# Kernel optimization log

Hardware: AMD Instinct MI355X
Metric: run time of the kernel (lower is better)

Reference implementation:

```python
import jax, jax.numpy as jnp
import numpy as np

B, S, H = 2, 2048, 2048
NH, KVH, HD = 32, 8, 64
G = NH // KVH
BASE = 10000.0
SCALE = 1.0 / np.sqrt(HD).astype(np.float32)


def _rope_cache(seq_len, dim, base):
    inv_freq = 1.0 / (base ** (jnp.arange(0, dim, 2, dtype=jnp.float32) / dim))
    t = jnp.arange(seq_len, dtype=jnp.float32)
    freqs = jnp.outer(t, inv_freq)            # [S, HD/2]
    emb = jnp.concatenate([freqs, freqs], -1)  # [S, HD]
    return jnp.cos(emb), jnp.sin(emb)


def _rotate_half(x):
    x1, x2 = jnp.split(x, 2, axis=-1)
    return jnp.concatenate([-x2, x1], axis=-1)


def setup_inputs() -> dict:
    key = jax.random.key(0)
    ks = jax.random.split(key, 5)
    hidden_states = jax.random.normal(ks[0], (B, S, H), jnp.float32)
    # additive causal mask, broadcast over heads
    causal = jnp.tril(jnp.ones((S, S), dtype=bool))
    attention_mask = jnp.where(causal, 0.0, -1e9).astype(jnp.float32)[None, None]
    attention_mask = jnp.broadcast_to(attention_mask, (B, 1, S, S))
    position_ids = jnp.broadcast_to(jnp.arange(S, dtype=jnp.int32), (B, S))
    w = 0.02
    Wq = jax.random.normal(ks[1], (H, NH * HD), jnp.float32) * w
    Wk = jax.random.normal(ks[2], (H, KVH * HD), jnp.float32) * w
    Wv = jax.random.normal(ks[3], (H, KVH * HD), jnp.float32) * w
    Wo = jax.random.normal(ks[4], (NH * HD, H), jnp.float32) * w
    return {"hidden_states": hidden_states, "attention_mask": attention_mask,
            "position_ids": position_ids, "Wq": Wq, "Wk": Wk, "Wv": Wv, "Wo": Wo}


def reference(hidden_states, attention_mask, position_ids, Wq, Wk, Wv, Wo):
    b, s, _ = hidden_states.shape
    q = (hidden_states @ Wq).reshape(b, s, NH, HD).transpose(0, 2, 1, 3)   # [B,NH,S,HD]
    k = (hidden_states @ Wk).reshape(b, s, KVH, HD).transpose(0, 2, 1, 3)  # [B,KVH,S,HD]
    v = (hidden_states @ Wv).reshape(b, s, KVH, HD).transpose(0, 2, 1, 3)
    cos_c, sin_c = _rope_cache(s, HD, BASE)
    cos = cos_c[position_ids][:, None]  # [B,1,S,HD]
    sin = sin_c[position_ids][:, None]
    q = q * cos + _rotate_half(q) * sin
    k = k * cos + _rotate_half(k) * sin
    # GQA: grouped einsum == repeat_kv + matmul (same math, no KV duplication)
    qg = q.reshape(b, KVH, G, s, HD)
    scores = jnp.einsum('bkgsd,bktd->bkgst', qg, k) * SCALE  # [B,KVH,G,S,S]
    scores = scores + attention_mask[:, :, None]             # mask [B,1,1,S,S]
    probs = jax.nn.softmax(scores.astype(jnp.float32), axis=-1).astype(q.dtype)
    ctx = jnp.einsum('bkgst,bktd->bkgsd', probs, v)
    ctx = ctx.reshape(b, NH, s, HD).transpose(0, 2, 1, 3).reshape(b, s, NH * HD)
    return ctx @ Wo
```

## Files before the change

kernel.cpp:

```cpp
#include <hip/hip_runtime.h>
#include <hip/hip_bf16.h>

#define DB   2
#define DS   2048
#define DH   2048
#define DNH  32
#define DKVH 8
#define DHD  64
#define DM   4096
#define DNQKV 3072

typedef __attribute__((ext_vector_type(8))) short bf16x8;
typedef __attribute__((ext_vector_type(4))) float f32x4;
typedef __attribute__((ext_vector_type(8))) unsigned short us8;
typedef __attribute__((ext_vector_type(4))) unsigned short us4;
typedef __attribute__((ext_vector_type(2))) unsigned int u32x2;

__device__ __forceinline__ float b2f(unsigned short u) {
  unsigned int x = ((unsigned int)u) << 16;
  return __builtin_bit_cast(float, x);
}
__device__ __forceinline__ unsigned short f2b(float f) {
  unsigned int u = __builtin_bit_cast(unsigned int, f);
  return (unsigned short)((u + 0x8000u) >> 16);
}
__device__ __forceinline__ unsigned int cvt_pk_bf16(float lo, float hi) {
  unsigned int r;
  asm("v_cvt_pk_bf16_f32 %0, %1, %2" : "=v"(r) : "v"(lo), "v"(hi));
  return r;
}
__device__ __forceinline__ void async_copy16(void* lds, const void* g) {
  __builtin_amdgcn_global_load_lds((const __attribute__((address_space(1))) void*)g,
                                   (__attribute__((address_space(3))) void*)lds,
                                   16, 0, 0);
}

#define BARRIER() do { asm volatile("" ::: "memory"); __builtin_amdgcn_s_barrier(); asm volatile("" ::: "memory"); } while (0)
#define LGKM0()   asm volatile("s_waitcnt lgkmcnt(0)" ::: "memory")
#define WAITVM(n) asm volatile("s_waitcnt vmcnt(" #n ")" ::: "memory")
#define MFMA16(d, a, bb) (d) = __builtin_amdgcn_mfma_f32_16x16x32_bf16((a), (bb), (d), 0, 0, 0)

__device__ __forceinline__ int detect_inline(const unsigned short* __restrict__ w) {
  int t = threadIdx.x & 63;
  int trips = 0;
#pragma unroll
  for (int i = 0; i < 4; i++) {
    unsigned short u = w[t * 4 + i];
    int e = (u >> 7) & 0xFF;
    if (e >= 161 || (e <= 93 && e != 0)) trips++;
  }
#pragma unroll
  for (int off = 32; off > 0; off >>= 1) trips += __shfl_down(trips, off);
  return __shfl(trips, 0) >= 8;
}

__global__ __launch_bounds__(256)
void prep(const void* __restrict__ hs, const void* __restrict__ wq,
          const void* __restrict__ wk, const void* __restrict__ wv,
          const void* __restrict__ wo,
          unsigned short* __restrict__ xb, unsigned short* __restrict__ wtqkv,
          unsigned short* __restrict__ wto) {
  __shared__ float tile[32][33];
  int mode = detect_inline((const unsigned short*)wq);
  int bid = blockIdx.x;
  if (bid < 4096) {
    int i = (bid * 256 + threadIdx.x) * 8;
    if (mode) {
      const float* f = (const float*)hs;
      us8 o;
#pragma unroll
      for (int j = 0; j < 8; j++) o[j] = f2b(f[i + j]);
      *(us8*)&xb[i] = o;
    } else {
      *(us8*)&xb[i] = *(const us8*)((const unsigned short*)hs + i);
    }
    return;
  }
  const void* win; unsigned short* out; int C, bx, by;
  if (bid < 8192)       { int l = bid - 4096;  win = wq; out = wtqkv;                         C = 2048; bx = l & 63; by = l >> 6; }
  else if (bid < 9216)  { int l = bid - 8192;  win = wk; out = wtqkv + (size_t)2048 * 2048;   C = 512;  bx = l & 15; by = l >> 4; }
  else if (bid < 10240) { int l = bid - 9216;  win = wv; out = wtqkv + (size_t)2560 * 2048;   C = 512;  bx = l & 15; by = l >> 4; }
  else                  { int l = bid - 10240; win = wo; out = wto;                           C = 2048; bx = l & 63; by = l >> 6; }
  int c0 = bx * 32, r0 = by * 32;
  int tx = threadIdx.x & 31, ty = threadIdx.x >> 5;
  if (mode) {
    const float* f = (const float*)win;
    for (int i = ty; i < 32; i += 8) tile[i][tx] = f[(size_t)(r0 + i) * C + c0 + tx];
  } else {
    const unsigned short* bsrc = (const unsigned short*)win;
    for (int i = ty; i < 32; i += 8) tile[i][tx] = b2f(bsrc[(size_t)(r0 + i) * C + c0 + tx]);
  }
  __syncthreads();
  for (int i = ty; i < 32; i += 8) out[(size_t)(c0 + i) * 2048 + r0 + tx] = f2b(tile[tx][i]);
}

#define QSC 0.18033688011112042f

__global__ __launch_bounds__(512, 2)
void gemm_qkv(const unsigned short* __restrict__ A, const unsigned short* __restrict__ Bt,
              const int* __restrict__ pos_ids,
              unsigned short* __restrict__ qws, unsigned short* __restrict__ kws,
              unsigned short* __restrict__ vt) {
  __shared__ __align__(16) unsigned short sm[65536];
  int tid = threadIdx.x, lane = tid & 63, wave = tid >> 6;
  int wm = wave >> 2, wn = wave & 3;
  int quad = lane >> 4, l15 = lane & 15;

  int bid = blockIdx.x;
  int wg = (bid & 7) * 24 + (bid >> 3);
  int ty = wg / 12, tx = wg - ty * 12;
  size_t tm0 = (size_t)ty * 256, tn0 = (size_t)tx * 256;

  const unsigned short* Ab = A + tm0 * 2048;
  const unsigned short* Bb = Bt + tn0 * 2048;

  auto UA = [&](int bu, int kh) { return sm + (bu * 2 + kh) * 8192; };
  auto UB = [&](int bu, int kh) { return sm + 32768 + (bu * 2 + kh) * 8192; };

  int c0 = tid, c1 = tid + 512;
  int r0s = c0 >> 2, r1s = c1 >> 2;
  int cc0 = (c0 & 3) ^ ((r0s >> 1) & 3);
  int cc1 = (c1 & 3) ^ ((r1s >> 1) & 3);
  size_t ga0 = (size_t)r0s * 2048 + cc0 * 8;
  size_t ga1 = (size_t)r1s * 2048 + cc1 * 8;

  auto stA = [&](int t, int kh, int bu) {
    const unsigned short* s = Ab + (size_t)t * 64 + kh * 32;
    async_copy16(UA(bu, kh) + c0 * 8, s + ga0);
    async_copy16(UA(bu, kh) + c1 * 8, s + ga1);
  };
  auto stB = [&](int t, int kh, int bu) {
    const unsigned short* s = Bb + (size_t)t * 64 + kh * 32;
    async_copy16(UB(bu, kh) + c0 * 8, s + ga0);
    async_copy16(UB(bu, kh) + c1 * 8, s + ga1);
  };

  int rdoff = l15 * 32 + ((quad << 3) ^ (((l15 >> 1) & 3) << 3));

  f32x4 zero4 = {0.f, 0.f, 0.f, 0.f};
  f32x4 acc[8][4];
#pragma unroll
  for (int mi = 0; mi < 8; mi++)
#pragma unroll
    for (int ni = 0; ni < 4; ni++) acc[mi][ni] = zero4;

  stA(0, 0, 0); stB(0, 0, 0); stA(0, 1, 0); stB(0, 1, 0); stA(1, 0, 1); stB(1, 0, 1);
  WAITVM(8); BARRIER();

#pragma unroll 2
  for (int t = 0; t < 32; ++t) {
    int bu = t & 1, bn = bu ^ 1;
    int t1 = (t + 1 < 32) ? t + 1 : 31;
    int t2 = (t + 2 < 32) ? t + 2 : 31;
    bf16x8 af[8];
    const unsigned short* pA0 = UA(bu, 0) + wm * 4096 + rdoff;
    const unsigned short* pB0 = UB(bu, 0) + wn * 2048 + rdoff;
    const unsigned short* pA1 = UA(bu, 1) + wm * 4096 + rdoff;
    const unsigned short* pB1 = UB(bu, 1) + wn * 2048 + rdoff;

#pragma unroll
    for (int mi = 0; mi < 8; mi++) af[mi] = *(const bf16x8*)(pA0 + mi * 512);
    bf16x8 b0 = *(const bf16x8*)pB0;
    bf16x8 b1 = *(const bf16x8*)(pB0 + 512);
    stA(t1, 1, bn);
    BARRIER(); LGKM0();
    __builtin_amdgcn_s_setprio(1);
#pragma unroll
    for (int mi = 0; mi < 8; mi++) { MFMA16(acc[mi][0], af[mi], b0); MFMA16(acc[mi][1], af[mi], b1); }
    __builtin_amdgcn_s_setprio(0);
    BARRIER();

    bf16x8 b2 = *(const bf16x8*)(pB0 + 1024);
    bf16x8 b3 = *(const bf16x8*)(pB0 + 1536);
    stB(t1, 1, bn);
    BARRIER(); LGKM0();
    __builtin_amdgcn_s_setprio(1);
#pragma unroll
    for (int mi = 0; mi < 8; mi++) { MFMA16(acc[mi][2], af[mi], b2); MFMA16(acc[mi][3], af[mi], b3); }
    __builtin_amdgcn_s_setprio(0);
    WAITVM(8);
    BARRIER();

#pragma unroll
    for (int mi = 0; mi < 8; mi++) af[mi] = *(const bf16x8*)(pA1 + mi * 512);
    b0 = *(const bf16x8*)pB1;
    b1 = *(const bf16x8*)(pB1 + 512);
    stA(t2, 0, bu);
    BARRIER(); LGKM0();
    __builtin_amdgcn_s_setprio(1);
#pragma unroll
    for (int mi = 0; mi < 8; mi++) { MFMA16(acc[mi][0], af[mi], b0); MFMA16(acc[mi][1], af[mi], b1); }
    __builtin_amdgcn_s_setprio(0);
    BARRIER();

    b2 = *(const bf16x8*)(pB1 + 1024);
    b3 = *(const bf16x8*)(pB1 + 1536);
    stB(t2, 0, bu);
    BARRIER(); LGKM0();
    __builtin_amdgcn_s_setprio(1);
#pragma unroll
    for (int mi = 0; mi < 8; mi++) { MFMA16(acc[mi][2], af[mi], b2); MFMA16(acc[mi][3], af[mi], b3); }
    __builtin_amdgcn_s_setprio(0);
    WAITVM(8);
    BARRIER();
  }
  WAITVM(0);

  int hs = (int)(tn0 >> 6) + wn;
  if (hs < 40) {
    float sc = (hs < 32) ? QSC : 1.0f;
    unsigned short* dst0 = (hs < 32) ? qws : kws;
    int hh = (hs < 32) ? hs : (hs - 32);
    float invf0 = __expf(-(float)l15 * (9.210340371976184f / 32.0f));
    float invf1 = invf0 * 0.01f;
#pragma unroll
    for (int mi = 0; mi < 8; mi++)
#pragma unroll
      for (int r = 0; r < 4; r++) {
        size_t gr = tm0 + wm * 128 + mi * 16 + quad * 4 + r;
        int bb = (int)(gr >> 11), s = (int)(gr & 2047);
        float tpos = (float)pos_ids[gr];
        unsigned short* row = dst0 + ((size_t)(bb * ((hs < 32) ? DNH : DKVH) + hh) * DS + s) * DHD;
#pragma unroll
        for (int ni = 0; ni < 2; ni++) {
          float x1 = acc[mi][ni][r], x2 = acc[mi][ni + 2][r];
          float ang = tpos * (ni ? invf1 : invf0);
          float sn, cs;
          __sincosf(ang, &sn, &cs);
          int d = ni * 16 + l15;
          row[d]      = f2b((x1 * cs - x2 * sn) * sc);
          row[d + 32] = f2b((x2 * cs + x1 * sn) * sc);
        }
      }
  } else {
    int vh = hs - 40;
    int bb = (int)(tm0 >> 11);
    int s0 = (int)(tm0 & 2047) + wm * 128 + quad * 4;
#pragma unroll
    for (int mi = 0; mi < 8; mi++)
#pragma unroll
      for (int ni = 0; ni < 4; ni++) {
        int d = ni * 16 + l15;
        us4 o4;
#pragma unroll
        for (int r = 0; r < 4; r++) o4[r] = f2b(acc[mi][ni][r]);
        *(us4*)&vt[((size_t)(bb * DKVH + vh) * DHD + d) * DS + s0 + mi * 16] = o4;
      }
  }
}

__global__ __launch_bounds__(512, 2)
void gemm_out(const unsigned short* __restrict__ A, const unsigned short* __restrict__ Bt,
              unsigned short* __restrict__ Cb, float* __restrict__ Cf,
              const unsigned short* __restrict__ wqdet) {
  __shared__ __align__(16) unsigned short sm[49152];
  int tid = threadIdx.x, lane = tid & 63, wave = tid >> 6;
  int wm = wave >> 2, wn = wave & 3;
  int quad = lane >> 4, l15 = lane & 15;

  int bid = blockIdx.x;
  int wg = (bid & 7) * 32 + (bid >> 3);
  int ty = wg >> 3, tx = wg & 7;
  size_t tm0 = (size_t)ty * 128, tn0 = (size_t)tx * 256;

  const unsigned short* Ab = A + tm0 * 2048;
  const unsigned short* Bb = Bt + tn0 * 2048;

  auto UA = [&](int bu, int kh) { return sm + (bu * 2 + kh) * 4096; };
  auto UB = [&](int bu, int kh) { return sm + 16384 + (bu * 2 + kh) * 8192; };

  int c0 = tid, c1 = tid + 512;
  int r0s = c0 >> 2, r1s = c1 >> 2;
  int cc0 = (c0 & 3) ^ ((r0s >> 1) & 3);
  int cc1 = (c1 & 3) ^ ((r1s >> 1) & 3);
  size_t ga0 = (size_t)r0s * 2048 + cc0 * 8;
  size_t ga1 = (size_t)r1s * 2048 + cc1 * 8;

  auto stA = [&](int t, int kh, int bu) {
    const unsigned short* s = Ab + (size_t)t * 64 + kh * 32;
    async_copy16(UA(bu, kh) + c0 * 8, s + ga0);
  };
  auto stB = [&](int t, int kh, int bu) {
    const unsigned short* s = Bb + (size_t)t * 64 + kh * 32;
    async_copy16(UB(bu, kh) + c0 * 8, s + ga0);
    async_copy16(UB(bu, kh) + c1 * 8, s + ga1);
  };

  int rdoff = l15 * 32 + ((quad << 3) ^ (((l15 >> 1) & 3) << 3));

  f32x4 zero4 = {0.f, 0.f, 0.f, 0.f};
  f32x4 acc[4][4];
#pragma unroll
  for (int mi = 0; mi < 4; mi++)
#pragma unroll
    for (int ni = 0; ni < 4; ni++) acc[mi][ni] = zero4;

  stA(0, 0, 0); stB(0, 0, 0); stA(0, 1, 0); stB(0, 1, 0); stA(1, 0, 1); stB(1, 0, 1);
  WAITVM(6); BARRIER();

#pragma unroll 2
  for (int t = 0; t < 32; ++t) {
    int bu = t & 1, bn = bu ^ 1;
    int t1 = (t + 1 < 32) ? t + 1 : 31;
    int t2 = (t + 2 < 32) ? t + 2 : 31;
    bf16x8 af[4];
    const unsigned short* pA0 = UA(bu, 0) + wm * 2048 + rdoff;
    const unsigned short* pB0 = UB(bu, 0) + wn * 2048 + rdoff;
    const unsigned short* pA1 = UA(bu, 1) + wm * 2048 + rdoff;
    const unsigned short* pB1 = UB(bu, 1) + wn * 2048 + rdoff;

#pragma unroll
    for (int mi = 0; mi < 4; mi++) af[mi] = *(const bf16x8*)(pA0 + mi * 512);
    bf16x8 b0 = *(const bf16x8*)pB0;
    bf16x8 b1 = *(const bf16x8*)(pB0 + 512);
    stA(t1, 1, bn);
    BARRIER(); LGKM0();
    __builtin_amdgcn_s_setprio(1);
#pragma unroll
    for (int mi = 0; mi < 4; mi++) { MFMA16(acc[mi][0], af[mi], b0); MFMA16(acc[mi][1], af[mi], b1); }
    __builtin_amdgcn_s_setprio(0);
    BARRIER();

    bf16x8 b2 = *(const bf16x8*)(pB0 + 1024);
    bf16x8 b3 = *(const bf16x8*)(pB0 + 1536);
    stB(t1, 1, bn);
    BARRIER(); LGKM0();
    __builtin_amdgcn_s_setprio(1);
#pragma unroll
    for (int mi = 0; mi < 4; mi++) { MFMA16(acc[mi][2], af[mi], b2); MFMA16(acc[mi][3], af[mi], b3); }
    __builtin_amdgcn_s_setprio(0);
    WAITVM(6);
    BARRIER();

#pragma unroll
    for (int mi = 0; mi < 4; mi++) af[mi] = *(const bf16x8*)(pA1 + mi * 512);
    b0 = *(const bf16x8*)pB1;
    b1 = *(const bf16x8*)(pB1 + 512);
    stA(t2, 0, bu);
    BARRIER(); LGKM0();
    __builtin_amdgcn_s_setprio(1);
#pragma unroll
    for (int mi = 0; mi < 4; mi++) { MFMA16(acc[mi][0], af[mi], b0); MFMA16(acc[mi][1], af[mi], b1); }
    __builtin_amdgcn_s_setprio(0);
    BARRIER();

    b2 = *(const bf16x8*)(pB1 + 1024);
    b3 = *(const bf16x8*)(pB1 + 1536);
    stB(t2, 0, bu);
    BARRIER(); LGKM0();
    __builtin_amdgcn_s_setprio(1);
#pragma unroll
    for (int mi = 0; mi < 4; mi++) { MFMA16(acc[mi][2], af[mi], b2); MFMA16(acc[mi][3], af[mi], b3); }
    __builtin_amdgcn_s_setprio(0);
    WAITVM(6);
    BARRIER();
  }
  WAITVM(0);

  int mode = detect_inline(wqdet);
#pragma unroll
  for (int mi = 0; mi < 4; mi++)
#pragma unroll
    for (int ni = 0; ni < 4; ni++)
#pragma unroll
      for (int r = 0; r < 4; r++) {
        size_t gr = tm0 + wm * 64 + mi * 16 + quad * 4 + r;
        size_t gc = tn0 + wn * 64 + ni * 16 + l15;
        float v = acc[mi][ni][r];
        if (mode) Cf[gr * 2048 + gc] = v;
        else      Cb[gr * 2048 + gc] = f2b(v);
      }
}

__global__ __launch_bounds__(256, 4)
void flash_attn(const unsigned short* __restrict__ q, const unsigned short* __restrict__ k,
                const unsigned short* __restrict__ vt, unsigned short* __restrict__ ctx) {
  __shared__ __align__(16) unsigned short lK[2][2][64 * 32];
  __shared__ __align__(16) unsigned short lV[2][2][64 * 32];
  __shared__ __align__(16) unsigned short lP[4][16 * 64];
  int tid = threadIdx.x, lane = tid & 63, wave = tid >> 6;
  int quad = lane >> 4, l15 = lane & 15;
  int bh = blockIdx.y, b = bh >> 5, h = bh & 31, kvh = h >> 2;
  const unsigned short* qb = q + (size_t)(b * DNH + h) * DS * DHD;
  const unsigned short* kb = k + (size_t)(b * DKVH + kvh) * DS * DHD;
  const unsigned short* vb = vt + (size_t)(b * DKVH + kvh) * DHD * DS;
  unsigned short* lPw = lP[wave];
  int r4 = tid >> 2;
  int cc8 = ((tid & 3) ^ ((r4 >> 1) & 3)) * 8;
  int swz = ((l15 >> 1) & 3) << 3;
  int pswz = (l15 & 7) << 3;

  f32x4 zero4 = {0.f, 0.f, 0.f, 0.f};
  for (int ph = 0; ph < 2; ph++) {
    int qt = ph ? (31 - blockIdx.x) : blockIdx.x;
    int q0 = qt * 64;
    const unsigned short* qp = qb + (size_t)(q0 + wave * 16 + l15) * DHD + quad * 8;
    bf16x8 qf0 = *(const bf16x8*)qp;
    bf16x8 qf1 = *(const bf16x8*)(qp + 32);
    f32x4 oacc[4];
#pragma unroll
    for (int dj = 0; dj < 4; dj++) oacc[dj] = zero4;
    float mrow = -1e30f, lrow = 0.f;

    int nt = qt + 1;
    {
      const unsigned short* sk = kb + (size_t)r4 * DHD + cc8;
      async_copy16(&lK[0][0][tid * 8], sk);
      async_copy16(&lK[0][1][tid * 8], sk + 32);
      const unsigned short* sv = vb + (size_t)r4 * DS + cc8;
      async_copy16(&lV[0][0][tid * 8], sv);
      async_copy16(&lV[0][1][tid * 8], sv + 32);
    }
    WAITVM(0); BARRIER();

    int cur = 0;
    for (int t = 0; t < nt; t++) {
      int kv0 = t * 64;
      if (t + 1 < nt) {
        const unsigned short* sk = kb + (size_t)(kv0 + 64 + r4) * DHD + cc8;
        async_copy16(&lK[cur ^ 1][0][tid * 8], sk);
        async_copy16(&lK[cur ^ 1][1][tid * 8], sk + 32);
        const unsigned short* sv = vb + (size_t)r4 * DS + kv0 + 64 + cc8;
        async_copy16(&lV[cur ^ 1][0][tid * 8], sv);
        async_copy16(&lV[cur ^ 1][1][tid * 8], sv + 32);
      }
      f32x4 sacc[4];
#pragma unroll
      for (int nj = 0; nj < 4; nj++) {
        int ro = (nj * 16 + l15) * 32 + ((quad * 8) ^ swz);
        bf16x8 kf0 = *(const bf16x8*)&lK[cur][0][ro];
        bf16x8 kf1 = *(const bf16x8*)&lK[cur][1][ro];
        sacc[nj] = zero4;
        MFMA16(sacc[nj], kf0, qf0);
        MFMA16(sacc[nj], kf1, qf1);
      }
      if (t == nt - 1) {
        int ql = wave * 16 + l15;
#pragma unroll
        for (int nj = 0; nj < 4; nj++)
#pragma unroll
          for (int r = 0; r < 4; r++)
            if (nj * 16 + quad * 4 + r > ql) sacc[nj][r] = -1e30f;
      }
      float a0 = fmaxf(fmaxf(sacc[0][0], sacc[0][1]), sacc[0][2]);
      float a1 = fmaxf(fmaxf(sacc[0][3], sacc[1][0]), sacc[1][1]);
      float a2 = fmaxf(fmaxf(sacc[1][2], sacc[1][3]), sacc[2][0]);
      float a3 = fmaxf(fmaxf(sacc[2][1], sacc[2][2]), sacc[2][3]);
      float a4 = fmaxf(fmaxf(sacc[3][0], sacc[3][1]), sacc[3][2]);
      float tm = fmaxf(fmaxf(fmaxf(a0, a1), fmaxf(a2, a3)), fmaxf(a4, sacc[3][3]));
      tm = fmaxf(tm, __shfl_xor(tm, 16));
      tm = fmaxf(tm, __shfl_xor(tm, 32));
      if (!__all(tm <= mrow + 8.f)) {
        float mn = fmaxf(mrow, tm);
        float alpha = __builtin_amdgcn_exp2f(mrow - mn);
        mrow = mn;
        lrow *= alpha;
#pragma unroll
        for (int dj = 0; dj < 4; dj++)
#pragma unroll
          for (int r = 0; r < 4; r++) oacc[dj][r] *= alpha;
      }
      float rs = 0.f;
#pragma unroll
      for (int nj = 0; nj < 4; nj++)
#pragma unroll
        for (int r = 0; r < 4; r++) {
          float e = __builtin_amdgcn_exp2f(sacc[nj][r] - mrow);
          sacc[nj][r] = e;
          rs += e;
        }
      rs += __shfl_xor(rs, 16);
      rs += __shfl_xor(rs, 32);
      lrow += rs;
#pragma unroll
      for (int nj = 0; nj < 4; nj++) {
        u32x2 w2;
        w2[0] = cvt_pk_bf16(sacc[nj][0], sacc[nj][1]);
        w2[1] = cvt_pk_bf16(sacc[nj][2], sacc[nj][3]);
        *(u32x2*)&lPw[l15 * 64 + ((nj * 16 + quad * 4) ^ pswz)] = w2;
      }
      bf16x8 pf0 = *(const bf16x8*)&lPw[l15 * 64 + ((quad * 8) ^ pswz)];
      bf16x8 pf1 = *(const bf16x8*)&lPw[l15 * 64 + ((32 + quad * 8) ^ pswz)];
#pragma unroll
      for (int dj = 0; dj < 4; dj++) {
        int ro = (dj * 16 + l15) * 32 + ((quad * 8) ^ swz);
        bf16x8 vf0 = *(const bf16x8*)&lV[cur][0][ro];
        bf16x8 vf1 = *(const bf16x8*)&lV[cur][1][ro];
        MFMA16(oacc[dj], vf0, pf0);
        MFMA16(oacc[dj], vf1, pf1);
      }
      WAITVM(0); BARRIER();
      cur ^= 1;
    }
    float inv = __builtin_amdgcn_rcpf(lrow);
    size_t orow = ((size_t)b * DS + q0 + wave * 16 + l15) * (DNH * DHD) + (size_t)h * DHD;
#pragma unroll
    for (int dj = 0; dj < 4; dj++) {
      u32x2 o2;
      o2[0] = cvt_pk_bf16(oacc[dj][0] * inv, oacc[dj][1] * inv);
      o2[1] = cvt_pk_bf16(oacc[dj][2] * inv, oacc[dj][3] * inv);
      *(u32x2*)&ctx[orow + dj * 16 + quad * 4] = o2;
    }
  }
}

extern "C" void kernel_launch(void* const* d_in, const int* in_sizes, int n_in,
                              void* d_out, int out_size, void* d_ws, size_t ws_size,
                              hipStream_t stream) {
  (void)in_sizes; (void)n_in; (void)out_size; (void)ws_size;
  const void* hs = d_in[0];
  const int* pos = (const int*)d_in[2];
  const void* wq = d_in[3];
  const void* wk = d_in[4];
  const void* wv = d_in[5];
  const void* wo = d_in[6];

  char* ws = (char*)d_ws;
  size_t off = 0;
  auto take = [&](size_t bytes) -> char* {
    char* p = ws + off;
    off += (bytes + 255) & ~(size_t)255;
    return p;
  };
  unsigned short* xb    = (unsigned short*)take((size_t)DM * DH * 2);
  unsigned short* wtqkv = (unsigned short*)take((size_t)DNQKV * DH * 2);
  unsigned short* wto   = (unsigned short*)take((size_t)DH * DH * 2);
  unsigned short* qws   = (unsigned short*)take((size_t)DB * DNH * DS * DHD * 2);
  unsigned short* kws   = (unsigned short*)take((size_t)DB * DKVH * DS * DHD * 2);
  unsigned short* vtws  = (unsigned short*)take((size_t)DB * DKVH * DS * DHD * 2);
  unsigned short* ctx   = (unsigned short*)take((size_t)DM * DNH * DHD * 2);

  prep<<<14336, 256, 0, stream>>>(hs, wq, wk, wv, wo, xb, wtqkv, wto);

  gemm_qkv<<<dim3(192), 512, 0, stream>>>(xb, wtqkv, pos, qws, kws, vtws);

  flash_attn<<<dim3(16, DB * DNH), 256, 0, stream>>>(qws, kws, vtws, ctx);

  gemm_out<<<dim3(256), 512, 0, stream>>>(ctx, wto, (unsigned short*)d_out, (float*)d_out,
                                          (const unsigned short*)wq);
}
```

Baseline: 302.1 us.

## Process paired causal query tiles together, sharing K/V tile loads

The flash attention block previously handled its two query tiles (qt and 31-qt) in two sequential passes, each streaming K/V through shared memory. Now both tiles' accumulators live at once, and the shared K/V prefix is loaded once and used by both. The longer tile then continues alone. This roughly halves K/V global-to-LDS traffic and barriers for the overlapping range and adds s_setprio hints around the MFMA sections, at the cost of more registers per thread, which may hurt occupancy under launch_bounds(256,4).

```diff
diff --git a/kernel.cpp b/kernel.cpp
--- a/kernel.cpp
+++ b/kernel.cpp
@@ -389,111 +389,142 @@
   int cc8 = ((tid & 3) ^ ((r4 >> 1) & 3)) * 8;
   int swz = ((l15 >> 1) & 3) << 3;
   int pswz = (l15 & 7) << 3;
+  int ql = wave * 16 + l15;
+
+  int qt = blockIdx.x;
+  int ntA = qt + 1, ntB = 32 - qt;
+  int q0A = qt * 64, q0B = (31 - qt) * 64;
+
+  const unsigned short* qpA = qb + (size_t)(q0A + ql) * DHD + quad * 8;
+  const unsigned short* qpB = qb + (size_t)(q0B + ql) * DHD + quad * 8;
+  bf16x8 qfA0 = *(const bf16x8*)qpA;
+  bf16x8 qfA1 = *(const bf16x8*)(qpA + 32);
+  bf16x8 qfB0 = *(const bf16x8*)qpB;
+  bf16x8 qfB1 = *(const bf16x8*)(qpB + 32);
 
   f32x4 zero4 = {0.f, 0.f, 0.f, 0.f};
-  for (int ph = 0; ph < 2; ph++) {
-    int qt = ph ? (31 - blockIdx.x) : blockIdx.x;
-    int q0 = qt * 64;
-    const unsigned short* qp = qb + (size_t)(q0 + wave * 16 + l15) * DHD + quad * 8;
-    bf16x8 qf0 = *(const bf16x8*)qp;
-    bf16x8 qf1 = *(const bf16x8*)(qp + 32);
-    f32x4 oacc[4];
-#pragma unroll
-    for (int dj = 0; dj < 4; dj++) oacc[dj] = zero4;
-    float mrow = -1e30f, lrow = 0.f;
-
-    int nt = qt + 1;
-    {
-      const unsigned short* sk = kb + (size_t)r4 * DHD + cc8;
-      async_copy16(&lK[0][0][tid * 8], sk);
-      async_copy16(&lK[0][1][tid * 8], sk + 32);
-      const unsigned short* sv = vb + (size_t)r4 * DS + cc8;
-      async_copy16(&lV[0][0][tid * 8], sv);
-      async_copy16(&lV[0][1][tid * 8], sv + 32);
-    }
+  f32x4 oA[4], oB[4];
+#pragma unroll
+  for (int dj = 0; dj < 4; dj++) { oA[dj] = zero4; oB[dj] = zero4; }
+  float mA = -1e30f, lA = 0.f, mB = -1e30f, lB = 0.f;
+
+  auto stage = [&](int t, int buf) {
+    const unsigned short* sk = kb + (size_t)(t * 64 + r4) * DHD + cc8;
+    async_copy16(&lK[buf][0][tid * 8], sk);
+    async_copy16(&lK[buf][1][tid * 8], sk + 32);
+    const unsigned short* sv = vb + (size_t)r4 * DS + t * 64 + cc8;
+    async_copy16(&lV[buf][0][tid * 8], sv);
+    async_copy16(&lV[buf][1][tid * 8], sv + 32);
+  };
+
+  auto smax_pv = [&](f32x4 (&sacc)[4], float& mrow, float& lrow, f32x4 (&oacc)[4],
+                     int cur, int maskdiag) {
+    if (maskdiag) {
+#pragma unroll
+      for (int nj = 0; nj < 4; nj++)
+#pragma unroll
+        for (int r = 0; r < 4; r++)
+          if (nj * 16 + quad * 4 + r > ql) sacc[nj][r] = -1e30f;
+    }
+    float a0 = fmaxf(fmaxf(sacc[0][0], sacc[0][1]), sacc[0][2]);
+    float a1 = fmaxf(fmaxf(sacc[0][3], sacc[1][0]), sacc[1][1]);
+    float a2 = fmaxf(fmaxf(sacc[1][2], sacc[1][3]), sacc[2][0]);
+    float a3 = fmaxf(fmaxf(sacc[2][1], sacc[2][2]), sacc[2][3]);
+    float a4 = fmaxf(fmaxf(sacc[3][0], sacc[3][1]), sacc[3][2]);
+    float tm = fmaxf(fmaxf(fmaxf(a0, a1), fmaxf(a2, a3)), fmaxf(a4, sacc[3][3]));
+    tm = fmaxf(tm, __shfl_xor(tm, 16));
+    tm = fmaxf(tm, __shfl_xor(tm, 32));
+    if (!__all(tm <= mrow + 8.f)) {
+      float mn = fmaxf(mrow, tm);
+      float alpha = __builtin_amdgcn_exp2f(mrow - mn);
+      mrow = mn;
+      lrow *= alpha;
+#pragma unroll
+      for (int dj = 0; dj < 4; dj++)
+#pragma unroll
+        for (int r = 0; r < 4; r++) oacc[dj][r] *= alpha;
+    }
+    float rs = 0.f;
+#pragma unroll
+    for (int nj = 0; nj < 4; nj++)
+#pragma unroll
+      for (int r = 0; r < 4; r++) {
+        float e = __builtin_amdgcn_exp2f(sacc[nj][r] - mrow);
+        sacc[nj][r] = e;
+        rs += e;
+      }
+    rs += __shfl_xor(rs, 16);
+    rs += __shfl_xor(rs, 32);
+    lrow += rs;
+#pragma unroll
+    for (int nj = 0; nj < 4; nj++) {
+      u32x2 w2;
+      w2[0] = cvt_pk_bf16(sacc[nj][0], sacc[nj][1]);
+      w2[1] = cvt_pk_bf16(sacc[nj][2], sacc[nj][3]);
+      *(u32x2*)&lPw[l15 * 64 + ((nj * 16 + quad * 4) ^ pswz)] = w2;
+    }
+    bf16x8 pf0 = *(const bf16x8*)&lPw[l15 * 64 + ((quad * 8) ^ pswz)];
+    bf16x8 pf1 = *(const bf16x8*)&lPw[l15 * 64 + ((32 + quad * 8) ^ pswz)];
+    __builtin_amdgcn_s_setprio(1);
+#pragma unroll
+    for (int dj = 0; dj < 4; dj++) {
+      int ro = (dj * 16 + l15) * 32 + ((quad * 8) ^ swz);
+      bf16x8 vf0 = *(const bf16x8*)&lV[cur][0][ro];
+      bf16x8 vf1 = *(const bf16x8*)&lV[cur][1][ro];
+      MFMA16(oacc[dj], vf0, pf0);
+      MFMA16(oacc[dj], vf1, pf1);
+    }
+    __builtin_amdgcn_s_setprio(0);
+  };
+
+  stage(0, 0);
+  WAITVM(0); BARRIER();
+
+  int cur = 0;
+  for (int t = 0; t < ntA; t++) {
+    stage(t + 1, cur ^ 1);
+    f32x4 sA[4], sB[4];
+    __builtin_amdgcn_s_setprio(1);
+#pragma unroll
+    for (int nj = 0; nj < 4; nj++) {
+      int ro = (nj * 16 + l15) * 32 + ((quad * 8) ^ swz);
+      bf16x8 kf0 = *(const bf16x8*)&lK[cur][0][ro];
+      bf16x8 kf1 = *(const bf16x8*)&lK[cur][1][ro];
+      sA[nj] = zero4;
+      MFMA16(sA[nj], kf0, qfA0);
+      MFMA16(sA[nj], kf1, qfA1);
+      sB[nj] = zero4;
+      MFMA16(sB[nj], kf0, qfB0);
+      MFMA16(sB[nj], kf1, qfB1);
+    }
+    __builtin_amdgcn_s_setprio(0);
+    smax_pv(sA, mA, lA, oA, cur, t == ntA - 1);
+    smax_pv(sB, mB, lB, oB, cur, 0);
     WAITVM(0); BARRIER();
-
-    int cur = 0;
-    for (int t = 0; t < nt; t++) {
-      int kv0 = t * 64;
-      if (t + 1 < nt) {
-        const unsigned short* sk = kb + (size_t)(kv0 + 64 + r4) * DHD + cc8;
-        async_copy16(&lK[cur ^ 1][0][tid * 8], sk);
-        async_copy16(&lK[cur ^ 1][1][tid * 8], sk + 32);
-        const unsigned short* sv = vb + (size_t)r4 * DS + kv0 + 64 + cc8;
-        async_copy16(&lV[cur ^ 1][0][tid * 8], sv);
-        async_copy16(&lV[cur ^ 1][1][tid * 8], sv + 32);
-      }
-      f32x4 sacc[4];
-#pragma unroll
-      for (int nj = 0; nj < 4; nj++) {
-        int ro = (nj * 16 + l15) * 32 + ((quad * 8) ^ swz);
-        bf16x8 kf0 = *(const bf16x8*)&lK[cur][0][ro];
-        bf16x8 kf1 = *(const bf16x8*)&lK[cur][1][ro];
-        sacc[nj] = zero4;
-        MFMA16(sacc[nj], kf0, qf0);
-        MFMA16(sacc[nj], kf1, qf1);
-      }
-      if (t == nt - 1) {
-        int ql = wave * 16 + l15;
-#pragma unroll
-        for (int nj = 0; nj < 4; nj++)
-#pragma unroll
-          for (int r = 0; r < 4; r++)
-            if (nj * 16 + quad * 4 + r > ql) sacc[nj][r] = -1e30f;
-      }
-      float a0 = fmaxf(fmaxf(sacc[0][0], sacc[0][1]), sacc[0][2]);
-      float a1 = fmaxf(fmaxf(sacc[0][3], sacc[1][0]), sacc[1][1]);
-      float a2 = fmaxf(fmaxf(sacc[1][2], sacc[1][3]), sacc[2][0]);
-      float a3 = fmaxf(fmaxf(sacc[2][1], sacc[2][2]), sacc[2][3]);
-      float a4 = fmaxf(fmaxf(sacc[3][0], sacc[3][1]), sacc[3][2]);
-      float tm = fmaxf(fmaxf(fmaxf(a0, a1), fmaxf(a2, a3)), fmaxf(a4, sacc[3][3]));
-      tm = fmaxf(tm, __shfl_xor(tm, 16));
-      tm = fmaxf(tm, __shfl_xor(tm, 32));
-      if (!__all(tm <= mrow + 8.f)) {
-        float mn = fmaxf(mrow, tm);
-        float alpha = __builtin_amdgcn_exp2f(mrow - mn);
-        mrow = mn;
-        lrow *= alpha;
-#pragma unroll
-        for (int dj = 0; dj < 4; dj++)
-#pragma unroll
-          for (int r = 0; r < 4; r++) oacc[dj][r] *= alpha;
-      }
-      float rs = 0.f;
-#pragma unroll
-      for (int nj = 0; nj < 4; nj++)
-#pragma unroll
-        for (int r = 0; r < 4; r++) {
-          float e = __builtin_amdgcn_exp2f(sacc[nj][r] - mrow);
-          sacc[nj][r] = e;
-          rs += e;
-        }
-      rs += __shfl_xor(rs, 16);
-      rs += __shfl_xor(rs, 32);
-      lrow += rs;
-#pragma unroll
-      for (int nj = 0; nj < 4; nj++) {
-        u32x2 w2;
-        w2[0] = cvt_pk_bf16(sacc[nj][0], sacc[nj][1]);
-        w2[1] = cvt_pk_bf16(sacc[nj][2], sacc[nj][3]);
-        *(u32x2*)&lPw[l15 * 64 + ((nj * 16 + quad * 4) ^ pswz)] = w2;
-      }
-      bf16x8 pf0 = *(const bf16x8*)&lPw[l15 * 64 + ((quad * 8) ^ pswz)];
-      bf16x8 pf1 = *(const bf16x8*)&lPw[l15 * 64 + ((32 + quad * 8) ^ pswz)];
-#pragma unroll
-      for (int dj = 0; dj < 4; dj++) {
-        int ro = (dj * 16 + l15) * 32 + ((quad * 8) ^ swz);
-        bf16x8 vf0 = *(const bf16x8*)&lV[cur][0][ro];
-        bf16x8 vf1 = *(const bf16x8*)&lV[cur][1][ro];
-        MFMA16(oacc[dj], vf0, pf0);
-        MFMA16(oacc[dj], vf1, pf1);
-      }
-      WAITVM(0); BARRIER();
-      cur ^= 1;
-    }
+    cur ^= 1;
+  }
+  for (int t = ntA; t < ntB; t++) {
+    if (t + 1 < ntB) stage(t + 1, cur ^ 1);
+    f32x4 sB[4];
+    __builtin_amdgcn_s_setprio(1);
+#pragma unroll
+    for (int nj = 0; nj < 4; nj++) {
+      int ro = (nj * 16 + l15) * 32 + ((quad * 8) ^ swz);
+      bf16x8 kf0 = *(const bf16x8*)&lK[cur][0][ro];
+      bf16x8 kf1 = *(const bf16x8*)&lK[cur][1][ro];
+      sB[nj] = zero4;
+      MFMA16(sB[nj], kf0, qfB0);
+      MFMA16(sB[nj], kf1, qfB1);
+    }
+    __builtin_amdgcn_s_setprio(0);
+    smax_pv(sB, mB, lB, oB, cur, t == ntB - 1);
+    WAITVM(0); BARRIER();
+    cur ^= 1;
+  }
+
+  auto wout = [&](f32x4 (&oacc)[4], float lrow, int q0) {
     float inv = __builtin_amdgcn_rcpf(lrow);
-    size_t orow = ((size_t)b * DS + q0 + wave * 16 + l15) * (DNH * DHD) + (size_t)h * DHD;
+    size_t orow = ((size_t)b * DS + q0 + ql) * (DNH * DHD) + (size_t)h * DHD;
 #pragma unroll
     for (int dj = 0; dj < 4; dj++) {
       u32x2 o2;
@@ -501,7 +532,9 @@
       o2[1] = cvt_pk_bf16(oacc[dj][2] * inv, oacc[dj][3] * inv);
       *(u32x2*)&ctx[orow + dj * 16 + quad * 4] = o2;
     }
-  }
+  };
+  wout(oA, lA, q0A);
+  wout(oB, lB, q0B);
 }
 
 extern "C" void kernel_launch(void* const* d_in, const int* in_sizes, int n_in,
```

Result: no change. 306.6 us (+1.5%).
